# Kernel optimization log

Measured on AMD Instinct MI355X. Metric: run time of the kernel, lower is better.

Reference implementation:

```python
import jax, jax.numpy as jnp
import numpy as np

HEAD_SIZE = 128
NUM_EMBED = 1024
BLOCK_SIZE = 2048


def setup_inputs() -> dict:
    key = jax.random.key(0)
    kx, kk, kq, kv = jax.random.split(key, 4)
    x = jax.random.normal(kx, (4, BLOCK_SIZE, NUM_EMBED), dtype=jnp.float32)
    s = 1.0 / np.sqrt(NUM_EMBED)
    Wk = jax.random.normal(kk, (NUM_EMBED, HEAD_SIZE), dtype=jnp.float32) * s
    Wq = jax.random.normal(kq, (NUM_EMBED, HEAD_SIZE), dtype=jnp.float32) * s
    Wv = jax.random.normal(kv, (NUM_EMBED, HEAD_SIZE), dtype=jnp.float32) * s
    return {"x": x, "Wk": Wk, "Wq": Wq, "Wv": Wv}


def reference(x, Wk, Wq, Wv):
    # x: [B, T, C]; W*: [C, H]
    B, T, C = x.shape
    k = x @ Wk          # [B, T, H]
    q = x @ Wq          # [B, T, H]
    v = x @ Wv          # [B, T, H]
    scale = k.shape[-1] ** -0.5
    wei = jnp.einsum('bth,bsh->bts', q, k) * scale  # [B, T, T]
    causal = jnp.tril(jnp.ones((T, T), dtype=bool))
    wei = jnp.where(causal, wei, -jnp.inf)
    wei = jax.nn.softmax(wei, axis=-1)
    out = jnp.einsum('bts,bsh->bth', wei, v)        # [B, T, H]
    return out
```

## Files before the change

### kernel.cpp

```cpp
#include <hip/hip_runtime.h>
#include <hip/hip_bf16.h>
#include <math.h>

#define B_ 4
#define T_ 2048
#define C_ 1024
#define H_ 128
#define SCALE 0.088388347648318447f

typedef unsigned short u16;
typedef __bf16 bf16x8 __attribute__((ext_vector_type(8)));
typedef __bf16 bf16x4 __attribute__((ext_vector_type(4)));
typedef float  f32x4  __attribute__((ext_vector_type(4)));
typedef u16    u16x8  __attribute__((ext_vector_type(8)));
typedef u16    u16x4  __attribute__((ext_vector_type(4)));

#define PO_OFF  0u
#define ML_OFF  18874368u
#define WBT_OFF 19169280u
#define QB_OFF  19955712u
#define KB_OFF  22052864u
#define VT_OFF  24150016u

__device__ __forceinline__ u16 f2bf(float f) {
    __hip_bfloat16 h = __float2bfloat16(f);
    return __builtin_bit_cast(u16, h);
}

__device__ __forceinline__ void load_lds16(const void* g, void* l) {
    __builtin_amdgcn_global_load_lds(
        (const __attribute__((address_space(1))) unsigned int*)g,
        (__attribute__((address_space(3))) unsigned int*)l, 16, 0, 0);
}

__global__ __launch_bounds__(256) void convert_w(const float* __restrict__ Wq,
                                                 const float* __restrict__ Wk,
                                                 const float* __restrict__ Wv,
                                                 u16* __restrict__ wbT) {
    const int id = blockIdx.x * 256 + threadIdx.x;
    const int s = id >> 17;
    const int r = id & 131071;
    const int k = r >> 7, n = r & 127;
    const float* W = (s == 0) ? Wq : (s == 1) ? Wk : Wv;
    float v = W[k * 128 + n];
    if (s == 0) v *= SCALE;
    wbT[(s << 17) + (n << 10) + k] = f2bf(v);
}

__global__ __launch_bounds__(256) void gemm_qkv(
    const float* __restrict__ x, const u16* __restrict__ wbT,
    u16* __restrict__ qb, u16* __restrict__ kb, u16* __restrict__ vT)
{
    __shared__ u16 xs[4096];
    __shared__ u16 ws[8192];

    const int tid = threadIdx.x;
    const int w = tid >> 6, lane = tid & 63, lg = lane >> 4, lr = lane & 15;
    const int wm = w >> 1, wn = w & 1;
    const int s = blockIdx.y;
    const int m0 = blockIdx.x * 64;
    const u16* wsrc = wbT + (s << 17);

    const int xrow = tid >> 2;
    const int xseg = tid & 3;

    f32x4 acc[2][4] = {};

    for (int k0 = 0; k0 < C_; k0 += 64) {
        const float4* xp = (const float4*)&x[(size_t)(m0 + xrow) * C_ + k0 + xseg * 16];
        const float4 f0 = xp[0], f1 = xp[1], f2 = xp[2], f3 = xp[3];

        __syncthreads();
#pragma unroll
        for (int i = 0; i < 4; ++i) {
            const unsigned o = (unsigned)(w * 4 + i) * 1024u + (unsigned)lane * 16u;
            const unsigned o2 = o ^ (((o >> 7) & 7u) << 4);
            const unsigned row = o2 >> 7, col = (o2 & 127u) >> 1;
            load_lds16(wsrc + (size_t)row * C_ + k0 + col, &ws[(w * 4 + i) * 512]);
        }
        {
            u16x8 lo, hi;
            lo[0] = f2bf(f0.x); lo[1] = f2bf(f0.y); lo[2] = f2bf(f0.z); lo[3] = f2bf(f0.w);
            lo[4] = f2bf(f1.x); lo[5] = f2bf(f1.y); lo[6] = f2bf(f1.z); lo[7] = f2bf(f1.w);
            hi[0] = f2bf(f2.x); hi[1] = f2bf(f2.y); hi[2] = f2bf(f2.z); hi[3] = f2bf(f2.w);
            hi[4] = f2bf(f3.x); hi[5] = f2bf(f3.y); hi[6] = f2bf(f3.z); hi[7] = f2bf(f3.w);
            const unsigned sw = ((unsigned)xrow & 7u) << 4;
            char* rb = (char*)xs + xrow * 128;
            *(u16x8*)(rb + (((unsigned)xseg * 32 + 0) ^ sw)) = lo;
            *(u16x8*)(rb + (((unsigned)xseg * 32 + 16) ^ sw)) = hi;
        }
        __syncthreads();

#pragma unroll
        for (int kc = 0; kc < 2; ++kc) {
            bf16x8 af[2], bfr[4];
#pragma unroll
            for (int mi = 0; mi < 2; ++mi) {
                const int row = wm * 32 + mi * 16 + lr;
                const unsigned byte = (unsigned)(kc * 64 + lg * 16) ^ (((unsigned)row & 7u) << 4);
                af[mi] = *(const bf16x8*)((const char*)xs + row * 128 + byte);
            }
#pragma unroll
            for (int ni = 0; ni < 4; ++ni) {
                const int n = wn * 64 + ni * 16 + lr;
                const unsigned byte = (unsigned)(kc * 64 + lg * 16) ^ (((unsigned)n & 7u) << 4);
                bfr[ni] = *(const bf16x8*)((const char*)ws + n * 128 + byte);
            }
#pragma unroll
            for (int mi = 0; mi < 2; ++mi)
#pragma unroll
                for (int ni = 0; ni < 4; ++ni)
                    acc[mi][ni] = __builtin_amdgcn_mfma_f32_16x16x32_bf16(
                        af[mi], bfr[ni], acc[mi][ni], 0, 0, 0);
        }
    }

    if (s < 2) {
        u16* dst = (s == 0) ? qb : kb;
#pragma unroll
        for (int mi = 0; mi < 2; ++mi)
#pragma unroll
            for (int ni = 0; ni < 4; ++ni) {
                const int trow = m0 + wm * 32 + mi * 16 + lg * 4;
                const int col = wn * 64 + ni * 16 + lr;
#pragma unroll
                for (int r = 0; r < 4; ++r)
                    dst[(size_t)(trow + r) * H_ + col] = f2bf(acc[mi][ni][r]);
            }
    } else {
#pragma unroll
        for (int mi = 0; mi < 2; ++mi)
#pragma unroll
            for (int ni = 0; ni < 4; ++ni) {
                const int trow = m0 + wm * 32 + mi * 16 + lg * 4;
                const int bb = trow >> 11, t = trow & 2047;
                const int d = wn * 64 + ni * 16 + lr;
                u16x4 pk;
                pk[0] = f2bf(acc[mi][ni][0]); pk[1] = f2bf(acc[mi][ni][1]);
                pk[2] = f2bf(acc[mi][ni][2]); pk[3] = f2bf(acc[mi][ni][3]);
                *(u16x4*)&vT[((size_t)bb * 128 + d) * 2048 + t] = pk;
            }
    }
}

__global__ __launch_bounds__(128) void attn_split(
    const u16* __restrict__ qb, const u16* __restrict__ kb,
    const u16* __restrict__ vT, float* __restrict__ po, float* __restrict__ ml)
{
    __shared__ u16 ks[2][4096];
    __shared__ u16 vs[2][128 * 36];

    const int jt = blockIdx.x, sp = blockIdx.y, b = blockIdx.z;
    if (sp * 8 > jt) return;
    const int kt0 = sp * 8;
    const int kt_end = min(kt0 + 8, jt + 1);

    const int tid = threadIdx.x;
    const int w = tid >> 6, lane = tid & 63, lg = lane >> 4, lr = lane & 15;
    const int qrow_base = jt * 32 + w * 16;

    const u16* kbB = kb + ((size_t)(b << 11)) * H_;
    const u16* vbB = vT + (size_t)b * 128 * 2048;

    unsigned krow[4], kcolb[4];
#pragma unroll
    for (int i = 0; i < 4; ++i) {
        const unsigned o_ = (unsigned)(w * 4 + i) * 1024u + (unsigned)lane * 16u;
        const unsigned o2 = o_ ^ (((o_ >> 8) & 7u) << 4);
        krow[i] = o2 >> 8; kcolb[i] = o2 & 255u;
    }
    int vd[4], vc[4];
#pragma unroll
    for (int i = 0; i < 4; ++i) {
        const int idx = i * 128 + tid;
        vd[i] = idx >> 2; vc[i] = idx & 3;
    }

    const u16* qp = qb + ((size_t)(b << 11) + qrow_base + lr) * H_;
    bf16x8 qf[4];
#pragma unroll
    for (int kc = 0; kc < 4; ++kc)
        qf[kc] = *(const bf16x8*)&qp[kc * 32 + lg * 8];

    u16x8 vr[4];
    {
        const u16* kbase = kbB + (size_t)kt0 * 32 * H_;
#pragma unroll
        for (int i = 0; i < 4; ++i)
            load_lds16((const char*)kbase + krow[i] * 256 + kcolb[i], &ks[0][(w * 4 + i) * 512]);
        const u16* vbase = vbB + (size_t)kt0 * 32;
#pragma unroll
        for (int i = 0; i < 4; ++i)
            vr[i] = *(const u16x8*)&vbase[(size_t)vd[i] * 2048 + vc[i] * 8];
#pragma unroll
        for (int i = 0; i < 4; ++i)
            *(u16x8*)((char*)vs[0] + vd[i] * 72 + vc[i] * 16) = vr[i];
    }
    __syncthreads();

    f32x4 o[8] = {};
    float m_run = -INFINITY, l_run = 0.f;
    int cur = 0;

    for (int kt = kt0; kt < kt_end; ++kt) {
        const bool pf = (kt + 1 < kt_end);
        if (pf) {
            const u16* kbase = kbB + (size_t)(kt + 1) * 32 * H_;
#pragma unroll
            for (int i = 0; i < 4; ++i)
                load_lds16((const char*)kbase + krow[i] * 256 + kcolb[i],
                           &ks[cur ^ 1][(w * 4 + i) * 512]);
            const u16* vbase = vbB + (size_t)(kt + 1) * 32;
#pragma unroll
            for (int i = 0; i < 4; ++i)
                vr[i] = *(const u16x8*)&vbase[(size_t)vd[i] * 2048 + vc[i] * 8];
        }

        f32x4 s0 = {0.f, 0.f, 0.f, 0.f}, s1 = {0.f, 0.f, 0.f, 0.f};
        const unsigned swz = ((unsigned)lr & 7u) << 4;
#pragma unroll
        for (int kc = 0; kc < 4; ++kc) {
            const unsigned byte = ((unsigned)(kc * 64 + lg * 16)) ^ swz;
            const bf16x8 kf0 = *(const bf16x8*)((const char*)ks[cur] + lr * 256 + byte);
            const bf16x8 kf1 = *(const bf16x8*)((const char*)ks[cur] + lr * 256 + 4096 + byte);
            s0 = __builtin_amdgcn_mfma_f32_16x16x32_bf16(kf0, qf[kc], s0, 0, 0, 0);
            s1 = __builtin_amdgcn_mfma_f32_16x16x32_bf16(kf1, qf[kc], s1, 0, 0, 0);
        }

        if (kt == jt) {
            const int qq = w * 16 + lr;
#pragma unroll
            for (int r = 0; r < 4; ++r) {
                if (lg * 4 + r > qq)      s0[r] = -INFINITY;
                if (16 + lg * 4 + r > qq) s1[r] = -INFINITY;
            }
        }

        float mt = fmaxf(fmaxf(fmaxf(s0[0], s0[1]), fmaxf(s0[2], s0[3])),
                         fmaxf(fmaxf(s1[0], s1[1]), fmaxf(s1[2], s1[3])));
        mt = fmaxf(mt, __shfl_xor(mt, 16));
        mt = fmaxf(mt, __shfl_xor(mt, 32));
        const float mn = fmaxf(m_run, mt);
        const float p0 = __expf(s0[0] - mn), p1 = __expf(s0[1] - mn);
        const float p2 = __expf(s0[2] - mn), p3 = __expf(s0[3] - mn);
        const float p4 = __expf(s1[0] - mn), p5 = __expf(s1[1] - mn);
        const float p6 = __expf(s1[2] - mn), p7 = __expf(s1[3] - mn);
        float sum = ((p0 + p1) + (p2 + p3)) + ((p4 + p5) + (p6 + p7));
        sum += __shfl_xor(sum, 16);
        sum += __shfl_xor(sum, 32);
        const float f = __expf(m_run - mn);
        l_run = l_run * f + sum;
        m_run = mn;

        const float fb0 = __shfl(f, lg * 4 + 0);
        const float fb1 = __shfl(f, lg * 4 + 1);
        const float fb2 = __shfl(f, lg * 4 + 2);
        const float fb3 = __shfl(f, lg * 4 + 3);
#pragma unroll
        for (int ni = 0; ni < 8; ++ni) {
            o[ni][0] *= fb0; o[ni][1] *= fb1; o[ni][2] *= fb2; o[ni][3] *= fb3;
        }

        bf16x8 pa;
        pa[0] = (__bf16)p0; pa[1] = (__bf16)p1; pa[2] = (__bf16)p2; pa[3] = (__bf16)p3;
        pa[4] = (__bf16)p4; pa[5] = (__bf16)p5; pa[6] = (__bf16)p6; pa[7] = (__bf16)p7;

#pragma unroll
        for (int ni = 0; ni < 8; ++ni) {
            const int n = ni * 16 + lr;
            const char* vrow = (const char*)vs[cur] + n * 72;
            const bf16x4 vlo = *(const bf16x4*)(vrow + lg * 8);
            const bf16x4 vhi = *(const bf16x4*)(vrow + 32 + lg * 8);
            bf16x8 vf;
            vf[0] = vlo[0]; vf[1] = vlo[1]; vf[2] = vlo[2]; vf[3] = vlo[3];
            vf[4] = vhi[0]; vf[5] = vhi[1]; vf[6] = vhi[2]; vf[7] = vhi[3];
            o[ni] = __builtin_amdgcn_mfma_f32_16x16x32_bf16(pa, vf, o[ni], 0, 0, 0);
        }

        if (pf) {
#pragma unroll
            for (int i = 0; i < 4; ++i)
                *(u16x8*)((char*)vs[cur ^ 1] + vd[i] * 72 + vc[i] * 16) = vr[i];
        }
        __syncthreads();
        cur ^= 1;
    }

    const int g = jt >> 3, rr = jt & 7;
    const int slot = (g + 1) * (4 * g + rr) + sp;
    float* pob = po + (size_t)(b * 288 + slot) * 32 * 128;
#pragma unroll
    for (int ni = 0; ni < 8; ++ni) {
        const int col = ni * 16 + lr;
#pragma unroll
        for (int rj = 0; rj < 4; ++rj)
            pob[(w * 16 + lg * 4 + rj) * 128 + col] = o[ni][rj];
    }
    if (lg == 0) {
        float* mlb = ml + (size_t)(b * 288 + slot) * 64;
        mlb[w * 16 + lr] = m_run;
        mlb[32 + w * 16 + lr] = l_run;
    }
}

__global__ __launch_bounds__(256) void attn_combine(
    const float* __restrict__ po, const float* __restrict__ ml,
    float* __restrict__ out)
{
    const int rid = (blockIdx.x << 3) + (threadIdx.x >> 5);
    const int b = blockIdx.y;
    const int d4 = (threadIdx.x & 31) * 4;
    const int jt = rid >> 5, row = rid & 31;
    const int g = jt >> 3, rr = jt & 7;
    const int slot0 = (g + 1) * (4 * g + rr);
    const int c = g + 1;

    float M = -INFINITY;
#pragma unroll
    for (int si = 0; si < 8; ++si)
        if (si < c) M = fmaxf(M, ml[(size_t)(b * 288 + slot0 + si) * 64 + row]);

    float L = 0.f;
    float a0 = 0.f, a1 = 0.f, a2 = 0.f, a3 = 0.f;
#pragma unroll
    for (int si = 0; si < 8; ++si) {
        if (si < c) {
            const float* mlb = ml + (size_t)(b * 288 + slot0 + si) * 64;
            const float wgt = __expf(mlb[row] - M);
            L += wgt * mlb[32 + row];
            const float4 t = *(const float4*)&po[((size_t)(b * 288 + slot0 + si) * 32 + row) * 128 + d4];
            a0 = fmaf(wgt, t.x, a0); a1 = fmaf(wgt, t.y, a1);
            a2 = fmaf(wgt, t.z, a2); a3 = fmaf(wgt, t.w, a3);
        }
    }
    const float inv = 1.f / L;
    *(float4*)&out[((size_t)(b << 11) + rid) * H_ + d4] =
        make_float4(a0 * inv, a1 * inv, a2 * inv, a3 * inv);
}

extern "C" void kernel_launch(void* const* d_in, const int* in_sizes, int n_in,
                              void* d_out, int out_size, void* d_ws, size_t ws_size,
                              hipStream_t stream) {
    const float* x  = (const float*)d_in[0];
    const float* Wk = (const float*)d_in[1];
    const float* Wq = (const float*)d_in[2];
    const float* Wv = (const float*)d_in[3];
    float* out = (float*)d_out;

    float* po = (float*)((char*)d_ws + PO_OFF);
    float* ml = (float*)((char*)d_ws + ML_OFF);
    u16* wbT  = (u16*)((char*)d_ws + WBT_OFF);
    u16* qb   = (u16*)((char*)d_ws + QB_OFF);
    u16* kb   = (u16*)((char*)d_ws + KB_OFF);
    u16* vT   = (u16*)((char*)d_ws + VT_OFF);

    convert_w<<<1536, 256, 0, stream>>>(Wq, Wk, Wv, wbT);
    gemm_qkv<<<dim3(128, 3), 256, 0, stream>>>(x, wbT, qb, kb, vT);
    attn_split<<<dim3(64, 8, 4), 128, 0, stream>>>(qb, kb, vT, po, ml);
    attn_combine<<<dim3(256, 4), 256, 0, stream>>>(po, ml, out);
}
```

Measured before the change: 64.61 us.

## Double-buffer QKV GEMM loads and widen attention query tiles to 64 rows

The QKV projection GEMM now double-buffers its x and W LDS tiles, prefetching the next k-slice while MFMAs run on the current one. This replaces the two barriers per iteration with one. The split attention kernel now uses 256 threads and 64 query rows per block, which halves the K/V tile loads per query row. It adds per-wave causal masking with a finite floor on the running max, and reorders V in LDS so each fragment is read with a single 8-element load. The combine kernel's slot indexing is updated to match the new 64-row partitions, at the cost of more LDS and possibly fewer resident blocks.

Measured after the change: 67.66 us. 1.05x slower.

```diff
diff --git a/kernel.cpp b/kernel.cpp
--- a/kernel.cpp
+++ b/kernel.cpp
@@ -51,8 +51,8 @@
     const float* __restrict__ x, const u16* __restrict__ wbT,
     u16* __restrict__ qb, u16* __restrict__ kb, u16* __restrict__ vT)
 {
-    __shared__ u16 xs[4096];
-    __shared__ u16 ws[8192];
+    __shared__ u16 xs[2][4096];
+    __shared__ u16 ws[2][8192];
 
     const int tid = threadIdx.x;
     const int w = tid >> 6, lane = tid & 63, lg = lane >> 4, lr = lane & 15;
@@ -63,33 +63,49 @@
 
     const int xrow = tid >> 2;
     const int xseg = tid & 3;
+    const float* xbase = x + (size_t)(m0 + xrow) * C_ + xseg * 16;
+    const unsigned xsw = ((unsigned)xrow & 7u) << 4;
+
+    unsigned wro[4], wco[4];
+#pragma unroll
+    for (int i = 0; i < 4; ++i) {
+        const unsigned o = (unsigned)(w * 4 + i) * 1024u + (unsigned)lane * 16u;
+        const unsigned o2 = o ^ (((o >> 7) & 7u) << 4);
+        wro[i] = o2 >> 7; wco[i] = (o2 & 127u) >> 1;
+    }
 
     f32x4 acc[2][4] = {};
 
+    {
+        const float4 f0 = ((const float4*)xbase)[0], f1 = ((const float4*)xbase)[1];
+        const float4 f2 = ((const float4*)xbase)[2], f3 = ((const float4*)xbase)[3];
+#pragma unroll
+        for (int i = 0; i < 4; ++i)
+            load_lds16(wsrc + (size_t)wro[i] * C_ + wco[i], &ws[0][(w * 4 + i) * 512]);
+        u16x8 lo, hi;
+        lo[0] = f2bf(f0.x); lo[1] = f2bf(f0.y); lo[2] = f2bf(f0.z); lo[3] = f2bf(f0.w);
+        lo[4] = f2bf(f1.x); lo[5] = f2bf(f1.y); lo[6] = f2bf(f1.z); lo[7] = f2bf(f1.w);
+        hi[0] = f2bf(f2.x); hi[1] = f2bf(f2.y); hi[2] = f2bf(f2.z); hi[3] = f2bf(f2.w);
+        hi[4] = f2bf(f3.x); hi[5] = f2bf(f3.y); hi[6] = f2bf(f3.z); hi[7] = f2bf(f3.w);
+        char* rb = (char*)xs[0] + xrow * 128;
+        *(u16x8*)(rb + (((unsigned)xseg * 32 + 0) ^ xsw)) = lo;
+        *(u16x8*)(rb + (((unsigned)xseg * 32 + 16) ^ xsw)) = hi;
+    }
+    __syncthreads();
+
+    int buf = 0;
     for (int k0 = 0; k0 < C_; k0 += 64) {
-        const float4* xp = (const float4*)&x[(size_t)(m0 + xrow) * C_ + k0 + xseg * 16];
-        const float4 f0 = xp[0], f1 = xp[1], f2 = xp[2], f3 = xp[3];
-
-        __syncthreads();
-#pragma unroll
-        for (int i = 0; i < 4; ++i) {
-            const unsigned o = (unsigned)(w * 4 + i) * 1024u + (unsigned)lane * 16u;
-            const unsigned o2 = o ^ (((o >> 7) & 7u) << 4);
-            const unsigned row = o2 >> 7, col = (o2 & 127u) >> 1;
-            load_lds16(wsrc + (size_t)row * C_ + k0 + col, &ws[(w * 4 + i) * 512]);
-        }
-        {
-            u16x8 lo, hi;
-            lo[0] = f2bf(f0.x); lo[1] = f2bf(f0.y); lo[2] = f2bf(f0.z); lo[3] = f2bf(f0.w);
-            lo[4] = f2bf(f1.x); lo[5] = f2bf(f1.y); lo[6] = f2bf(f1.z); lo[7] = f2bf(f1.w);
-            hi[0] = f2bf(f2.x); hi[1] = f2bf(f2.y); hi[2] = f2bf(f2.z); hi[3] = f2bf(f2.w);
-            hi[4] = f2bf(f3.x); hi[5] = f2bf(f3.y); hi[6] = f2bf(f3.z); hi[7] = f2bf(f3.w);
-            const unsigned sw = ((unsigned)xrow & 7u) << 4;
-            char* rb = (char*)xs + xrow * 128;
-            *(u16x8*)(rb + (((unsigned)xseg * 32 + 0) ^ sw)) = lo;
-            *(u16x8*)(rb + (((unsigned)xseg * 32 + 16) ^ sw)) = hi;
-        }
-        __syncthreads();
+        const bool pf = (k0 + 64 < C_);
+        float4 g0, g1, g2, g3;
+        if (pf) {
+            const float* xn = xbase + k0 + 64;
+            g0 = ((const float4*)xn)[0]; g1 = ((const float4*)xn)[1];
+            g2 = ((const float4*)xn)[2]; g3 = ((const float4*)xn)[3];
+#pragma unroll
+            for (int i = 0; i < 4; ++i)
+                load_lds16(wsrc + (size_t)wro[i] * C_ + (k0 + 64) + wco[i],
+                           &ws[buf ^ 1][(w * 4 + i) * 512]);
+        }
 
 #pragma unroll
         for (int kc = 0; kc < 2; ++kc) {
@@ -98,13 +114,13 @@
             for (int mi = 0; mi < 2; ++mi) {
                 const int row = wm * 32 + mi * 16 + lr;
                 const unsigned byte = (unsigned)(kc * 64 + lg * 16) ^ (((unsigned)row & 7u) << 4);
-                af[mi] = *(const bf16x8*)((const char*)xs + row * 128 + byte);
+                af[mi] = *(const bf16x8*)((const char*)xs[buf] + row * 128 + byte);
             }
 #pragma unroll
             for (int ni = 0; ni < 4; ++ni) {
                 const int n = wn * 64 + ni * 16 + lr;
                 const unsigned byte = (unsigned)(kc * 64 + lg * 16) ^ (((unsigned)n & 7u) << 4);
-                bfr[ni] = *(const bf16x8*)((const char*)ws + n * 128 + byte);
+                bfr[ni] = *(const bf16x8*)((const char*)ws[buf] + n * 128 + byte);
             }
 #pragma unroll
             for (int mi = 0; mi < 2; ++mi)
@@ -113,6 +129,19 @@
                     acc[mi][ni] = __builtin_amdgcn_mfma_f32_16x16x32_bf16(
                         af[mi], bfr[ni], acc[mi][ni], 0, 0, 0);
         }
+
+        if (pf) {
+            u16x8 lo, hi;
+            lo[0] = f2bf(g0.x); lo[1] = f2bf(g0.y); lo[2] = f2bf(g0.z); lo[3] = f2bf(g0.w);
+            lo[4] = f2bf(g1.x); lo[5] = f2bf(g1.y); lo[6] = f2bf(g1.z); lo[7] = f2bf(g1.w);
+            hi[0] = f2bf(g2.x); hi[1] = f2bf(g2.y); hi[2] = f2bf(g2.z); hi[3] = f2bf(g2.w);
+            hi[4] = f2bf(g3.x); hi[5] = f2bf(g3.y); hi[6] = f2bf(g3.z); hi[7] = f2bf(g3.w);
+            char* rb = (char*)xs[buf ^ 1] + xrow * 128;
+            *(u16x8*)(rb + (((unsigned)xseg * 32 + 0) ^ xsw)) = lo;
+            *(u16x8*)(rb + (((unsigned)xseg * 32 + 16) ^ xsw)) = hi;
+        }
+        __syncthreads();
+        buf ^= 1;
     }
 
     if (s < 2) {
@@ -143,7 +172,7 @@
     }
 }
 
-__global__ __launch_bounds__(128) void attn_split(
+__global__ __launch_bounds__(256) void attn_split(
     const u16* __restrict__ qb, const u16* __restrict__ kb,
     const u16* __restrict__ vT, float* __restrict__ po, float* __restrict__ ml)
 {
@@ -151,28 +180,29 @@
     __shared__ u16 vs[2][128 * 36];
 
     const int jt = blockIdx.x, sp = blockIdx.y, b = blockIdx.z;
-    if (sp * 8 > jt) return;
     const int kt0 = sp * 8;
-    const int kt_end = min(kt0 + 8, jt + 1);
+    const int ktend_all = 2 * jt + 2;
+    if (kt0 >= ktend_all) return;
+    const int kt_end = min(kt0 + 8, ktend_all);
 
     const int tid = threadIdx.x;
     const int w = tid >> 6, lane = tid & 63, lg = lane >> 4, lr = lane & 15;
-    const int qrow_base = jt * 32 + w * 16;
+    const int qrow_base = jt * 64 + w * 16;
 
     const u16* kbB = kb + ((size_t)(b << 11)) * H_;
     const u16* vbB = vT + (size_t)b * 128 * 2048;
 
-    unsigned krow[4], kcolb[4];
-#pragma unroll
-    for (int i = 0; i < 4; ++i) {
-        const unsigned o_ = (unsigned)(w * 4 + i) * 1024u + (unsigned)lane * 16u;
+    unsigned krow[2], kcolb[2];
+#pragma unroll
+    for (int i = 0; i < 2; ++i) {
+        const unsigned o_ = (unsigned)(w * 2 + i) * 1024u + (unsigned)lane * 16u;
         const unsigned o2 = o_ ^ (((o_ >> 8) & 7u) << 4);
         krow[i] = o2 >> 8; kcolb[i] = o2 & 255u;
     }
-    int vd[4], vc[4];
-#pragma unroll
-    for (int i = 0; i < 4; ++i) {
-        const int idx = i * 128 + tid;
+    int vd[2], vc[2];
+#pragma unroll
+    for (int i = 0; i < 2; ++i) {
+        const int idx = i * 256 + tid;
         vd[i] = idx >> 2; vc[i] = idx & 3;
     }
 
@@ -182,19 +212,22 @@
     for (int kc = 0; kc < 4; ++kc)
         qf[kc] = *(const bf16x8*)&qp[kc * 32 + lg * 8];
 
-    u16x8 vr[4];
+    u16x8 vr[2];
     {
         const u16* kbase = kbB + (size_t)kt0 * 32 * H_;
 #pragma unroll
-        for (int i = 0; i < 4; ++i)
-            load_lds16((const char*)kbase + krow[i] * 256 + kcolb[i], &ks[0][(w * 4 + i) * 512]);
+        for (int i = 0; i < 2; ++i)
+            load_lds16((const char*)kbase + krow[i] * 256 + kcolb[i], &ks[0][(w * 2 + i) * 512]);
         const u16* vbase = vbB + (size_t)kt0 * 32;
 #pragma unroll
-        for (int i = 0; i < 4; ++i)
+        for (int i = 0; i < 2; ++i)
             vr[i] = *(const u16x8*)&vbase[(size_t)vd[i] * 2048 + vc[i] * 8];
 #pragma unroll
-        for (int i = 0; i < 4; ++i)
-            *(u16x8*)((char*)vs[0] + vd[i] * 72 + vc[i] * 16) = vr[i];
+        for (int i = 0; i < 2; ++i) {
+            char* rb = (char*)vs[0] + vd[i] * 72 + (vc[i] & 2) * 4;
+            *(u16x4*)(rb + ((2 * vc[i]) & 3) * 16)     = __builtin_shufflevector(vr[i], vr[i], 0, 1, 2, 3);
+            *(u16x4*)(rb + ((2 * vc[i] + 1) & 3) * 16) = __builtin_shufflevector(vr[i], vr[i], 4, 5, 6, 7);
+        }
     }
     __syncthreads();
 
@@ -207,12 +240,12 @@
         if (pf) {
             const u16* kbase = kbB + (size_t)(kt + 1) * 32 * H_;
 #pragma unroll
-            for (int i = 0; i < 4; ++i)
+            for (int i = 0; i < 2; ++i)
                 load_lds16((const char*)kbase + krow[i] * 256 + kcolb[i],
-                           &ks[cur ^ 1][(w * 4 + i) * 512]);
+                           &ks[cur ^ 1][(w * 2 + i) * 512]);
             const u16* vbase = vbB + (size_t)(kt + 1) * 32;
 #pragma unroll
-            for (int i = 0; i < 4; ++i)
+            for (int i = 0; i < 2; ++i)
                 vr[i] = *(const u16x8*)&vbase[(size_t)vd[i] * 2048 + vc[i] * 8];
         }
 
@@ -227,12 +260,13 @@
             s1 = __builtin_amdgcn_mfma_f32_16x16x32_bf16(kf1, qf[kc], s1, 0, 0, 0);
         }
 
-        if (kt == jt) {
-            const int qq = w * 16 + lr;
+        if (kt * 32 + 31 > qrow_base) {
+            const int qg = qrow_base + lr;
+            const int kvb = kt * 32 + lg * 4;
 #pragma unroll
             for (int r = 0; r < 4; ++r) {
-                if (lg * 4 + r > qq)      s0[r] = -INFINITY;
-                if (16 + lg * 4 + r > qq) s1[r] = -INFINITY;
+                if (kvb + r > qg)      s0[r] = -INFINITY;
+                if (kvb + 16 + r > qg) s1[r] = -INFINITY;
             }
         }
 
@@ -240,7 +274,7 @@
                          fmaxf(fmaxf(s1[0], s1[1]), fmaxf(s1[2], s1[3])));
         mt = fmaxf(mt, __shfl_xor(mt, 16));
         mt = fmaxf(mt, __shfl_xor(mt, 32));
-        const float mn = fmaxf(m_run, mt);
+        const float mn = fmaxf(fmaxf(m_run, mt), -1e30f);
         const float p0 = __expf(s0[0] - mn), p1 = __expf(s0[1] - mn);
         const float p2 = __expf(s0[2] - mn), p3 = __expf(s0[3] - mn);
         const float p4 = __expf(s1[0] - mn), p5 = __expf(s1[1] - mn);
@@ -267,28 +301,25 @@
 
 #pragma unroll
         for (int ni = 0; ni < 8; ++ni) {
-            const int n = ni * 16 + lr;
-            const char* vrow = (const char*)vs[cur] + n * 72;
-            const bf16x4 vlo = *(const bf16x4*)(vrow + lg * 8);
-            const bf16x4 vhi = *(const bf16x4*)(vrow + 32 + lg * 8);
-            bf16x8 vf;
-            vf[0] = vlo[0]; vf[1] = vlo[1]; vf[2] = vlo[2]; vf[3] = vlo[3];
-            vf[4] = vhi[0]; vf[5] = vhi[1]; vf[6] = vhi[2]; vf[7] = vhi[3];
+            const bf16x8 vf = *(const bf16x8*)((const char*)vs[cur] + (ni * 16 + lr) * 72 + lg * 16);
             o[ni] = __builtin_amdgcn_mfma_f32_16x16x32_bf16(pa, vf, o[ni], 0, 0, 0);
         }
 
         if (pf) {
 #pragma unroll
-            for (int i = 0; i < 4; ++i)
-                *(u16x8*)((char*)vs[cur ^ 1] + vd[i] * 72 + vc[i] * 16) = vr[i];
+            for (int i = 0; i < 2; ++i) {
+                char* rb = (char*)vs[cur ^ 1] + vd[i] * 72 + (vc[i] & 2) * 4;
+                *(u16x4*)(rb + ((2 * vc[i]) & 3) * 16)     = __builtin_shufflevector(vr[i], vr[i], 0, 1, 2, 3);
+                *(u16x4*)(rb + ((2 * vc[i] + 1) & 3) * 16) = __builtin_shufflevector(vr[i], vr[i], 4, 5, 6, 7);
+            }
         }
         __syncthreads();
         cur ^= 1;
     }
 
-    const int g = jt >> 3, rr = jt & 7;
-    const int slot = (g + 1) * (4 * g + rr) + sp;
-    float* pob = po + (size_t)(b * 288 + slot) * 32 * 128;
+    const int a = jt >> 2, b3 = jt & 3;
+    const int slot = (a + 1) * (2 * a + b3) + sp;
+    float* pob = po + (size_t)(b * 144 + slot) * 64 * 128;
 #pragma unroll
     for (int ni = 0; ni < 8; ++ni) {
         const int col = ni * 16 + lr;
@@ -297,9 +328,9 @@
             pob[(w * 16 + lg * 4 + rj) * 128 + col] = o[ni][rj];
     }
     if (lg == 0) {
-        float* mlb = ml + (size_t)(b * 288 + slot) * 64;
+        float* mlb = ml + (size_t)(b * 144 + slot) * 128;
         mlb[w * 16 + lr] = m_run;
-        mlb[32 + w * 16 + lr] = l_run;
+        mlb[64 + w * 16 + lr] = l_run;
     }
 }
 
@@ -310,25 +341,25 @@
     const int rid = (blockIdx.x << 3) + (threadIdx.x >> 5);
     const int b = blockIdx.y;
     const int d4 = (threadIdx.x & 31) * 4;
-    const int jt = rid >> 5, row = rid & 31;
-    const int g = jt >> 3, rr = jt & 7;
-    const int slot0 = (g + 1) * (4 * g + rr);
-    const int c = g + 1;
+    const int jt = rid >> 6, row = rid & 63;
+    const int a = jt >> 2, b3 = jt & 3;
+    const int slot0 = (a + 1) * (2 * a + b3);
+    const int c = a + 1;
 
     float M = -INFINITY;
 #pragma unroll
     for (int si = 0; si < 8; ++si)
-        if (si < c) M = fmaxf(M, ml[(size_t)(b * 288 + slot0 + si) * 64 + row]);
+        if (si < c) M = fmaxf(M, ml[(size_t)(b * 144 + slot0 + si) * 128 + row]);
 
     float L = 0.f;
     float a0 = 0.f, a1 = 0.f, a2 = 0.f, a3 = 0.f;
 #pragma unroll
     for (int si = 0; si < 8; ++si) {
         if (si < c) {
-            const float* mlb = ml + (size_t)(b * 288 + slot0 + si) * 64;
+            const float* mlb = ml + (size_t)(b * 144 + slot0 + si) * 128;
             const float wgt = __expf(mlb[row] - M);
-            L += wgt * mlb[32 + row];
-            const float4 t = *(const float4*)&po[((size_t)(b * 288 + slot0 + si) * 32 + row) * 128 + d4];
+            L += wgt * mlb[64 + row];
+            const float4 t = *(const float4*)&po[((size_t)(b * 144 + slot0 + si) * 64 + row) * 128 + d4];
             a0 = fmaf(wgt, t.x, a0); a1 = fmaf(wgt, t.y, a1);
             a2 = fmaf(wgt, t.z, a2); a3 = fmaf(wgt, t.w, a3);
         }
@@ -356,6 +387,6 @@
 
     convert_w<<<1536, 256, 0, stream>>>(Wq, Wk, Wv, wbT);
     gemm_qkv<<<dim3(128, 3), 256, 0, stream>>>(x, wbT, qb, kb, vT);
-    attn_split<<<dim3(64, 8, 4), 128, 0, stream>>>(qb, kb, vT, po, ml);
+    attn_split<<<dim3(32, 8, 4), 256, 0, stream>>>(qb, kb, vT, po, ml);
     attn_combine<<<dim3(256, 4), 256, 0, stream>>>(po, ml, out);
 }
```
